# Kernel tuning notes

Measured on AMD Instinct MI355X. Metric: run time of the kernel, lower is better.

## Reference

```python
import jax, jax.numpy as jnp
import numpy as np

NUM_HEADS = 16  # from init_kwargs


def setup_inputs() -> dict:
    key = jax.random.key(0)
    k1, k2, k3, k4, k5 = jax.random.split(key, 5)
    B, N, C = 2, 2048, 1024
    return {
        "query": jax.random.normal(k1, (B, N, C), dtype=jnp.float32),
        "key": jax.random.normal(k2, (B, N, C), dtype=jnp.float32),
        "value": jax.random.normal(k3, (B, N, C), dtype=jnp.float32),
        "W_merge": jax.random.normal(k4, (C, C), dtype=jnp.float32) * (1.0 / np.sqrt(C)),
        "b_merge": jax.random.normal(k5, (C,), dtype=jnp.float32) * 0.02,
    }


def reference(query, key, value, W_merge, b_merge):
    B, N, C = query.shape
    H = NUM_HEADS
    dim = C // H
    # Faithful to torch: plain reshape (B,N,C) -> (B, dim, H, N), no transpose.
    q = query.reshape(B, dim, H, -1)
    k = key.reshape(B, dim, H, -1)
    v = value.reshape(B, dim, H, -1)
    # Faithful scale: divide by sqrt(N) (sequence length), as in the source.
    scale = 1.0 / np.sqrt(N).astype(np.float32)
    scores = jnp.einsum('bdhn,bdhm->bhnm', q, k) * scale  # [B,H,N,N]
    attn = jax.nn.softmax(scores, axis=-1)
    x = jnp.einsum('bhnm,bdhm->bdhn', attn, v)  # [B,dim,H,N]
    x = x.reshape(B, C, -1)  # [B,C,N]
    # Conv1d(C,C,kernel_size=1) == pointwise channel matmul + bias
    out = jnp.einsum('oc,bcn->bon', W_merge, x) + b_merge[None, :, None]
    return out  # [B,C,N]
```

## Files before the change

### kernel.cpp

```cpp
#include <hip/hip_runtime.h>


#define H 16
#define DIM 64
#define NSEQ 2048
#define CCH 1024
#define BATCH 2
#define DSTR (H * NSEQ)

typedef __attribute__((ext_vector_type(8))) short bf16x8;
typedef __attribute__((ext_vector_type(4))) float f32x4;

__device__ __forceinline__ unsigned short f2bf(float x) {
  unsigned int u = __builtin_bit_cast(unsigned int, x);
  u += 0x7FFFu + ((u >> 16) & 1u);
  return (unsigned short)(u >> 16);
}

__device__ __forceinline__ void gld16(const void* g, void* l) {
  __builtin_amdgcn_global_load_lds(
      (const __attribute__((address_space(1))) unsigned int*)g,
      (__attribute__((address_space(3))) unsigned int*)l, 16, 0, 0);
}

__global__ __launch_bounds__(256) void prep_w(const float* __restrict__ W,
                                              unsigned short* __restrict__ Wp) {
  int idx = blockIdx.x * 256 + threadIdx.x;
  int o = idx >> 10, cp = idx & 1023;
  int hh = cp >> 6, d = cp & 63;
  Wp[idx] = f2bf(W[o * CCH + d * H + hh]);
}

__global__ __launch_bounds__(256) void conv_v(const float* __restrict__ v,
                                              unsigned short* __restrict__ Vb) {
  int idx = blockIdx.x * 256 + threadIdx.x;
  float4 x = ((const float4*)v)[idx];
  ushort4 o;
  o.x = f2bf(x.x); o.y = f2bf(x.y); o.z = f2bf(x.z); o.w = f2bf(x.w);
  ((ushort4*)Vb)[idx] = o;
}

__global__ __launch_bounds__(256) void prep_tr(const float* __restrict__ q,
                                               const float* __restrict__ k,
                                               unsigned short* __restrict__ Qt,
                                               unsigned short* __restrict__ Kt) {
  __shared__ unsigned short T[64][72];
  const int tid = threadIdx.x;
  const int n0 = blockIdx.x * 64;
  const int hh = blockIdx.y;
  const int b = blockIdx.z >> 1, t = blockIdx.z & 1;
  const float* src = t ? k : q;
  unsigned short* dst = t ? Kt : Qt;
  const float scl = t ? 1.0f : 0.022097086912079608f;
  const size_t base = (size_t)b * (CCH * NSEQ) + (size_t)hh * NSEQ;
#pragma unroll
  for (int it = 0; it < 4; ++it) {
    int i4 = it * 256 + tid;
    int d = i4 >> 4;
    int nn = (i4 & 15) << 2;
    float4 val = *(const float4*)(src + base + (size_t)d * DSTR + n0 + nn);
    T[nn + 0][d] = f2bf(val.x * scl);
    T[nn + 1][d] = f2bf(val.y * scl);
    T[nn + 2][d] = f2bf(val.z * scl);
    T[nn + 3][d] = f2bf(val.w * scl);
  }
  __syncthreads();
  const size_t obase = ((size_t)(b * H + hh) * NSEQ + n0) * 64;
#pragma unroll
  for (int it = 0; it < 2; ++it) {
    int idx = it * 256 + tid;
    int row = idx >> 3, cb = idx & 7;
    *(bf16x8*)(dst + obase + (size_t)row * 64 + cb * 8) = *(const bf16x8*)&T[row][cb * 8];
  }
}

__global__ __launch_bounds__(256) void attn2(const unsigned short* __restrict__ Qt,
                                             const unsigned short* __restrict__ Kt,
                                             const unsigned short* __restrict__ Vb,
                                             unsigned short* __restrict__ xt) {
  __shared__ unsigned short Qs[128 * 64];
  __shared__ unsigned short Ks[2][64 * 64];
  __shared__ unsigned short Vs[2][64 * 64];
  __shared__ unsigned short Ps[4][32][72];

  const int tid = threadIdx.x;
  const int w = tid >> 6, lane = tid & 63;
  const int quad = lane >> 4, l16 = lane & 15;
  const int n0 = blockIdx.x * 128;
  const int hh = blockIdx.y, b = blockIdx.z;

  const unsigned short* Qbase = Qt + ((size_t)(b * H + hh) * NSEQ + n0) * 64;
  const unsigned short* Kbase = Kt + ((size_t)(b * H + hh) * NSEQ) * 64;
  const unsigned short* Vbase = Vb + (size_t)b * (CCH * NSEQ) + (size_t)hh * NSEQ;

  const int srow = w * 8 + (lane >> 3);
  const int scb = lane & 7;

#pragma unroll
  for (int i = 0; i < 4; ++i) {
    int row = i * 32 + srow;
    int cbl = scb ^ (row & 7);
    gld16(Qbase + (size_t)row * 64 + cbl * 8, &Qs[(i * 32 + w * 8) * 64]);
  }
#pragma unroll
  for (int i = 0; i < 2; ++i) {
    int row = i * 32 + srow;
    int cbl = scb ^ (row & 7);
    gld16(Kbase + (size_t)row * 64 + cbl * 8, &Ks[0][(i * 32 + w * 8) * 64]);
    gld16(Vbase + (size_t)row * DSTR + cbl * 8, &Vs[0][(i * 32 + w * 8) * 64]);
  }
  __syncthreads();

  bf16x8 aQ[2][2];
#pragma unroll
  for (int nt = 0; nt < 2; ++nt)
#pragma unroll
    for (int kh = 0; kh < 2; ++kh) {
      int row = w * 32 + nt * 16 + l16;
      int phys = (kh * 4 + quad) ^ (l16 & 7);
      aQ[nt][kh] = *(const bf16x8*)&Qs[(size_t)row * 64 + phys * 8];
    }

  f32x4 O[2][4];
  float lsum[2][4];
#pragma unroll
  for (int nt = 0; nt < 2; ++nt) {
#pragma unroll
    for (int dt = 0; dt < 4; ++dt) O[nt][dt] = (f32x4){0.f, 0.f, 0.f, 0.f};
#pragma unroll
    for (int r = 0; r < 4; ++r) lsum[nt][r] = 0.f;
  }

  for (int it = 0; it < 32; ++it) {
    const int cur = it & 1;
    if (it + 1 < 32) {
      const int nxt = cur ^ 1;
      const int m0n = (it + 1) * 64;
#pragma unroll
      for (int i = 0; i < 2; ++i) {
        int row = i * 32 + srow;
        int cbl = scb ^ (row & 7);
        gld16(Kbase + (size_t)(m0n + row) * 64 + cbl * 8, &Ks[nxt][(i * 32 + w * 8) * 64]);
        gld16(Vbase + (size_t)row * DSTR + m0n + cbl * 8, &Vs[nxt][(i * 32 + w * 8) * 64]);
      }
    }

    f32x4 S[2][4];
#pragma unroll
    for (int nt = 0; nt < 2; ++nt)
#pragma unroll
      for (int ms = 0; ms < 4; ++ms) S[nt][ms] = (f32x4){0.f, 0.f, 0.f, 0.f};
#pragma unroll
    for (int ms = 0; ms < 4; ++ms)
#pragma unroll
      for (int kh = 0; kh < 2; ++kh) {
        int row = ms * 16 + l16;
        int phys = (kh * 4 + quad) ^ (l16 & 7);
        bf16x8 bK = *(const bf16x8*)&Ks[cur][(size_t)row * 64 + phys * 8];
        S[0][ms] = __builtin_amdgcn_mfma_f32_16x16x32_bf16(aQ[0][kh], bK, S[0][ms], 0, 0, 0);
        S[1][ms] = __builtin_amdgcn_mfma_f32_16x16x32_bf16(aQ[1][kh], bK, S[1][ms], 0, 0, 0);
      }

#pragma unroll
    for (int nt = 0; nt < 2; ++nt)
#pragma unroll
      for (int ms = 0; ms < 4; ++ms)
#pragma unroll
        for (int r = 0; r < 4; ++r) {
          float e = __expf(S[nt][ms][r]);
          lsum[nt][r] += e;
          Ps[w][nt * 16 + quad * 4 + r][ms * 16 + l16] = f2bf(e);
        }

    bf16x8 aP[2][2];
#pragma unroll
    for (int nt = 0; nt < 2; ++nt)
#pragma unroll
      for (int kh = 0; kh < 2; ++kh)
        aP[nt][kh] = *(const bf16x8*)&Ps[w][nt * 16 + l16][kh * 32 + quad * 8];
#pragma unroll
    for (int dt = 0; dt < 4; ++dt)
#pragma unroll
      for (int kh = 0; kh < 2; ++kh) {
        int row = dt * 16 + l16;
        int phys = (kh * 4 + quad) ^ (l16 & 7);
        bf16x8 bV = *(const bf16x8*)&Vs[cur][(size_t)row * 64 + phys * 8];
        O[0][dt] = __builtin_amdgcn_mfma_f32_16x16x32_bf16(aP[0][kh], bV, O[0][dt], 0, 0, 0);
        O[1][dt] = __builtin_amdgcn_mfma_f32_16x16x32_bf16(aP[1][kh], bV, O[1][dt], 0, 0, 0);
      }

    __syncthreads();
  }

#pragma unroll
  for (int nt = 0; nt < 2; ++nt)
#pragma unroll
    for (int r = 0; r < 4; ++r) {
#pragma unroll
      for (int off = 1; off < 16; off <<= 1)
        lsum[nt][r] += __shfl_xor(lsum[nt][r], off, 64);
    }

  const size_t xb = (size_t)b * ((size_t)NSEQ * CCH);
#pragma unroll
  for (int nt = 0; nt < 2; ++nt)
#pragma unroll
    for (int r = 0; r < 4; ++r) {
      float inv = 1.0f / lsum[nt][r];
      int n = n0 + w * 32 + nt * 16 + quad * 4 + r;
#pragma unroll
      for (int dt = 0; dt < 4; ++dt) {
        int cp = hh * 64 + dt * 16 + l16;
        xt[xb + (size_t)n * CCH + cp] = f2bf(O[nt][dt][r] * inv);
      }
    }
}

__global__ __launch_bounds__(256) void merge2(const unsigned short* __restrict__ Wp,
                                              const unsigned short* __restrict__ xt,
                                              const float* __restrict__ bias,
                                              float* __restrict__ out) {
  __shared__ unsigned short At[128 * 64];
  __shared__ unsigned short Bt[128 * 64];
  const int tid = threadIdx.x;
  const int w = tid >> 6, lane = tid & 63;
  const int quad = lane >> 4, l16 = lane & 15;
  const int wx = w & 1, wy = w >> 1;
  const int n0 = blockIdx.x * 128, o0 = blockIdx.y * 128, b = blockIdx.z;
  const int srow = w * 8 + (lane >> 3), scb = lane & 7;
  const unsigned short* Bbase = xt + (size_t)b * ((size_t)NSEQ * CCH);

  f32x4 acc[4][4];
#pragma unroll
  for (int ot = 0; ot < 4; ++ot)
#pragma unroll
    for (int nt = 0; nt < 4; ++nt) acc[ot][nt] = (f32x4){0.f, 0.f, 0.f, 0.f};

  for (int c0 = 0; c0 < CCH; c0 += 64) {
    __syncthreads();
#pragma unroll
    for (int i = 0; i < 4; ++i) {
      int row = i * 32 + srow;
      int cbl = scb ^ (row & 7);
      gld16(Wp + (size_t)(o0 + row) * CCH + c0 + cbl * 8, &At[(i * 32 + w * 8) * 64]);
      gld16(Bbase + (size_t)(n0 + row) * CCH + c0 + cbl * 8, &Bt[(i * 32 + w * 8) * 64]);
    }
    __syncthreads();
#pragma unroll
    for (int ks = 0; ks < 2; ++ks) {
      bf16x8 aW[4], bX[4];
      int phys = ((ks * 4 + quad) ^ (l16 & 7)) * 8;
#pragma unroll
      for (int t = 0; t < 4; ++t) {
        aW[t] = *(const bf16x8*)&At[(wy * 64 + t * 16 + l16) * 64 + phys];
        bX[t] = *(const bf16x8*)&Bt[(wx * 64 + t * 16 + l16) * 64 + phys];
      }
#pragma unroll
      for (int ot = 0; ot < 4; ++ot)
#pragma unroll
        for (int nt = 0; nt < 4; ++nt)
          acc[ot][nt] = __builtin_amdgcn_mfma_f32_16x16x32_bf16(aW[ot], bX[nt], acc[ot][nt], 0, 0, 0);
    }
  }

#pragma unroll
  for (int ot = 0; ot < 4; ++ot)
#pragma unroll
    for (int r = 0; r < 4; ++r) {
      int o = o0 + wy * 64 + ot * 16 + quad * 4 + r;
      float bi = bias[o];
#pragma unroll
      for (int nt = 0; nt < 4; ++nt)
        out[(size_t)b * ((size_t)CCH * NSEQ) + (size_t)o * NSEQ + n0 + wx * 64 + nt * 16 + l16] =
            acc[ot][nt][r] + bi;
    }
}

extern "C" void kernel_launch(void* const* d_in, const int* in_sizes, int n_in,
                              void* d_out, int out_size, void* d_ws, size_t ws_size,
                              hipStream_t stream) {
  const float* q = (const float*)d_in[0];
  const float* k = (const float*)d_in[1];
  const float* v = (const float*)d_in[2];
  const float* W = (const float*)d_in[3];
  const float* bias = (const float*)d_in[4];
  float* out = (float*)d_out;

  unsigned short* Wp = (unsigned short*)d_ws;
  unsigned short* xt = Wp + (1u << 20);
  unsigned short* Qt = xt + (4u << 20);
  unsigned short* Kt = Qt + (4u << 20);
  unsigned short* Vb = Kt + (4u << 20);

  hipLaunchKernelGGL(prep_w, dim3(4096), dim3(256), 0, stream, W, Wp);
  hipLaunchKernelGGL(conv_v, dim3(4096), dim3(256), 0, stream, v, Vb);
  hipLaunchKernelGGL(prep_tr, dim3(NSEQ / 64, H, BATCH * 2), dim3(256), 0, stream,
                     q, k, Qt, Kt);
  hipLaunchKernelGGL(attn2, dim3(NSEQ / 128, H, BATCH), dim3(256), 0, stream,
                     Qt, Kt, Vb, xt);
  hipLaunchKernelGGL(merge2, dim3(NSEQ / 128, CCH / 128, BATCH), dim3(256), 0, stream,
                     Wp, xt, bias, out);
}
```

Before: 199.0 us.

## Transpose score MFMA, fold log2e into Q scale, pack P stores, alias Q/P LDS

```diff
diff --git a/kernel.cpp b/kernel.cpp
--- a/kernel.cpp
+++ b/kernel.cpp
@@ -7,6 +7,7 @@
 #define CCH 1024
 #define BATCH 2
 #define DSTR (H * NSEQ)
+#define PSP 72
 
 typedef __attribute__((ext_vector_type(8))) short bf16x8;
 typedef __attribute__((ext_vector_type(4))) float f32x4;
@@ -15,6 +16,28 @@
   unsigned int u = __builtin_bit_cast(unsigned int, x);
   u += 0x7FFFu + ((u >> 16) & 1u);
   return (unsigned short)(u >> 16);
+}
+
+__device__ __forceinline__ unsigned int pack2bf(float a, float b) {
+#if __has_builtin(__builtin_amdgcn_cvt_pk_bf16_f32)
+  typedef __attribute__((ext_vector_type(2))) __bf16 bf16x2_t;
+  bf16x2_t r = __builtin_amdgcn_cvt_pk_bf16_f32(a, b);
+  return __builtin_bit_cast(unsigned int, r);
+#else
+  unsigned int ua = __builtin_bit_cast(unsigned int, a);
+  unsigned int ub = __builtin_bit_cast(unsigned int, b);
+  ua += 0x7FFFu + ((ua >> 16) & 1u);
+  ub += 0x7FFFu + ((ub >> 16) & 1u);
+  return __builtin_amdgcn_perm(ub, ua, 0x07060302u);
+#endif
+}
+
+__device__ __forceinline__ float fast_exp2(float x) {
+#if __has_builtin(__builtin_amdgcn_exp2f)
+  return __builtin_amdgcn_exp2f(x);
+#else
+  return exp2f(x);
+#endif
 }
 
 __device__ __forceinline__ void gld16(const void* g, void* l) {
@@ -51,7 +74,7 @@
   const int b = blockIdx.z >> 1, t = blockIdx.z & 1;
   const float* src = t ? k : q;
   unsigned short* dst = t ? Kt : Qt;
-  const float scl = t ? 1.0f : 0.022097086912079608f;
+  const float scl = t ? 1.0f : (0.022097086912079608f * 1.4426950408889634f);
   const size_t base = (size_t)b * (CCH * NSEQ) + (size_t)hh * NSEQ;
 #pragma unroll
   for (int it = 0; it < 4; ++it) {
@@ -74,14 +97,15 @@
   }
 }
 
-__global__ __launch_bounds__(256) void attn2(const unsigned short* __restrict__ Qt,
+__global__ __launch_bounds__(256) void attn3(const unsigned short* __restrict__ Qt,
                                              const unsigned short* __restrict__ Kt,
                                              const unsigned short* __restrict__ Vb,
                                              unsigned short* __restrict__ xt) {
-  __shared__ unsigned short Qs[128 * 64];
-  __shared__ unsigned short Ks[2][64 * 64];
-  __shared__ unsigned short Vs[2][64 * 64];
-  __shared__ unsigned short Ps[4][32][72];
+  __shared__ __align__(16) unsigned short Ks[2][64 * 64];
+  __shared__ __align__(16) unsigned short Vs[2][64 * 64];
+  __shared__ __align__(16) unsigned short UQ[4 * 32 * PSP];
+  unsigned short* Qs = UQ;
+  unsigned short* Ps = UQ;
 
   const int tid = threadIdx.x;
   const int w = tid >> 6, lane = tid & 63;
@@ -111,25 +135,25 @@
   }
   __syncthreads();
 
-  bf16x8 aQ[2][2];
+  bf16x8 bQ[2][2];
 #pragma unroll
   for (int nt = 0; nt < 2; ++nt)
 #pragma unroll
     for (int kh = 0; kh < 2; ++kh) {
       int row = w * 32 + nt * 16 + l16;
       int phys = (kh * 4 + quad) ^ (l16 & 7);
-      aQ[nt][kh] = *(const bf16x8*)&Qs[(size_t)row * 64 + phys * 8];
-    }
+      bQ[nt][kh] = *(const bf16x8*)&Qs[(size_t)row * 64 + phys * 8];
+    }
+  __syncthreads();
 
   f32x4 O[2][4];
-  float lsum[2][4];
-#pragma unroll
-  for (int nt = 0; nt < 2; ++nt) {
+  float lsum[2] = {0.f, 0.f};
+#pragma unroll
+  for (int nt = 0; nt < 2; ++nt)
 #pragma unroll
     for (int dt = 0; dt < 4; ++dt) O[nt][dt] = (f32x4){0.f, 0.f, 0.f, 0.f};
-#pragma unroll
-    for (int r = 0; r < 4; ++r) lsum[nt][r] = 0.f;
-  }
+
+  const int psw = w * 32 * PSP;
 
   for (int it = 0; it < 32; ++it) {
     const int cur = it & 1;
@@ -145,39 +169,44 @@
       }
     }
 
-    f32x4 S[2][4];
+    f32x4 St[4][2];
+#pragma unroll
+    for (int mt = 0; mt < 4; ++mt)
+#pragma unroll
+      for (int nt = 0; nt < 2; ++nt) St[mt][nt] = (f32x4){0.f, 0.f, 0.f, 0.f};
+#pragma unroll
+    for (int mt = 0; mt < 4; ++mt)
+#pragma unroll
+      for (int kh = 0; kh < 2; ++kh) {
+        int row = mt * 16 + l16;
+        int phys = (kh * 4 + quad) ^ (l16 & 7);
+        bf16x8 aK = *(const bf16x8*)&Ks[cur][(size_t)row * 64 + phys * 8];
+        St[mt][0] = __builtin_amdgcn_mfma_f32_16x16x32_bf16(aK, bQ[0][kh], St[mt][0], 0, 0, 0);
+        St[mt][1] = __builtin_amdgcn_mfma_f32_16x16x32_bf16(aK, bQ[1][kh], St[mt][1], 0, 0, 0);
+      }
+
+#pragma unroll
+    for (int nt = 0; nt < 2; ++nt) {
+#pragma unroll
+      for (int mt = 0; mt < 4; ++mt) {
+        float e0 = fast_exp2(St[mt][nt][0]);
+        float e1 = fast_exp2(St[mt][nt][1]);
+        float e2 = fast_exp2(St[mt][nt][2]);
+        float e3 = fast_exp2(St[mt][nt][3]);
+        lsum[nt] += (e0 + e1) + (e2 + e3);
+        uint2 pk;
+        pk.x = pack2bf(e0, e1);
+        pk.y = pack2bf(e2, e3);
+        *(uint2*)&Ps[psw + (nt * 16 + l16) * PSP + mt * 16 + quad * 4] = pk;
+      }
+    }
+
+    bf16x8 aP[2][2];
 #pragma unroll
     for (int nt = 0; nt < 2; ++nt)
 #pragma unroll
-      for (int ms = 0; ms < 4; ++ms) S[nt][ms] = (f32x4){0.f, 0.f, 0.f, 0.f};
-#pragma unroll
-    for (int ms = 0; ms < 4; ++ms)
-#pragma unroll
-      for (int kh = 0; kh < 2; ++kh) {
-        int row = ms * 16 + l16;
-        int phys = (kh * 4 + quad) ^ (l16 & 7);
-        bf16x8 bK = *(const bf16x8*)&Ks[cur][(size_t)row * 64 + phys * 8];
-        S[0][ms] = __builtin_amdgcn_mfma_f32_16x16x32_bf16(aQ[0][kh], bK, S[0][ms], 0, 0, 0);
-        S[1][ms] = __builtin_amdgcn_mfma_f32_16x16x32_bf16(aQ[1][kh], bK, S[1][ms], 0, 0, 0);
-      }
-
-#pragma unroll
-    for (int nt = 0; nt < 2; ++nt)
-#pragma unroll
-      for (int ms = 0; ms < 4; ++ms)
-#pragma unroll
-        for (int r = 0; r < 4; ++r) {
-          float e = __expf(S[nt][ms][r]);
-          lsum[nt][r] += e;
-          Ps[w][nt * 16 + quad * 4 + r][ms * 16 + l16] = f2bf(e);
-        }
-
-    bf16x8 aP[2][2];
-#pragma unroll
-    for (int nt = 0; nt < 2; ++nt)
-#pragma unroll
       for (int kh = 0; kh < 2; ++kh)
-        aP[nt][kh] = *(const bf16x8*)&Ps[w][nt * 16 + l16][kh * 32 + quad * 8];
+        aP[nt][kh] = *(const bf16x8*)&Ps[psw + (nt * 16 + l16) * PSP + kh * 32 + quad * 8];
 #pragma unroll
     for (int dt = 0; dt < 4; ++dt)
 #pragma unroll
@@ -193,20 +222,17 @@
   }
 
 #pragma unroll
+  for (int nt = 0; nt < 2; ++nt) {
+    lsum[nt] += __shfl_xor(lsum[nt], 16, 64);
+    lsum[nt] += __shfl_xor(lsum[nt], 32, 64);
+  }
+
+  const size_t xb = (size_t)b * ((size_t)NSEQ * CCH);
+#pragma unroll
   for (int nt = 0; nt < 2; ++nt)
 #pragma unroll
     for (int r = 0; r < 4; ++r) {
-#pragma unroll
-      for (int off = 1; off < 16; off <<= 1)
-        lsum[nt][r] += __shfl_xor(lsum[nt][r], off, 64);
-    }
-
-  const size_t xb = (size_t)b * ((size_t)NSEQ * CCH);
-#pragma unroll
-  for (int nt = 0; nt < 2; ++nt)
-#pragma unroll
-    for (int r = 0; r < 4; ++r) {
-      float inv = 1.0f / lsum[nt][r];
+      float inv = 1.0f / __shfl(lsum[nt], quad * 4 + r, 64);
       int n = n0 + w * 32 + nt * 16 + quad * 4 + r;
 #pragma unroll
       for (int dt = 0; dt < 4; ++dt) {
@@ -296,7 +322,7 @@
   hipLaunchKernelGGL(conv_v, dim3(4096), dim3(256), 0, stream, v, Vb);
   hipLaunchKernelGGL(prep_tr, dim3(NSEQ / 64, H, BATCH * 2), dim3(256), 0, stream,
                      q, k, Qt, Kt);
-  hipLaunchKernelGGL(attn2, dim3(NSEQ / 128, H, BATCH), dim3(256), 0, stream,
+  hipLaunchKernelGGL(attn3, dim3(NSEQ / 128, H, BATCH), dim3(256), 0, stream,
                      Qt, Kt, Vb, xt);
   hipLaunchKernelGGL(merge2, dim3(NSEQ / 128, CCH / 128, BATCH), dim3(256), 0, stream,
                      Wp, xt, bias, out);
```

After: 191.6 us. -3.7%, faster.
